# Optimization experiments

Hardware: AMD Instinct MI355X
Metric: run time of the kernel (lower is better)

## Reference

```python
import jax, jax.numpy as jnp
import numpy as np
from jax import lax

B, NP = 4, 8192          # events, points per event (equal-sized batches)
RATIO, R, K = 0.25, 0.2, 64
MP = int(NP * RATIO)     # sampled centers per event
D_IN = 32
BIG = 1e10


def _fps_one(pos):
    # Farthest point sampling (deterministic start at index 0). pos: [NP,3] -> [MP] int32
    d = jnp.sum((pos - pos[0]) ** 2, axis=-1)
    sel = jnp.zeros((MP,), jnp.int32)

    def body(i, carry):
        sel, d = carry
        nxt = jnp.argmax(d).astype(jnp.int32)
        sel = sel.at[i].set(nxt)
        d = jnp.minimum(d, jnp.sum((pos - pos[nxt]) ** 2, axis=-1))
        return sel, d

    sel, _ = lax.fori_loop(1, MP, body, (sel, d))
    return sel


def _ball_query_one(centers, pos):
    # centers: [MP,3], pos: [NP,3] -> neighbor idx [MP,K] int32, validity mask [MP,K]
    d2 = jnp.sum((centers[:, None, :] - pos[None, :, :]) ** 2, axis=-1)  # [MP,NP]
    d2m = jnp.where(d2 <= R * R, d2, BIG)
    neg, idx = lax.top_k(-d2m, K)          # K nearest within radius (deterministic)
    mask = (-neg) <= R * R
    return idx.astype(jnp.int32), mask


def reference(x, pos, batch, W1, b1, W2, b2, W3, b3):
    xb = x.reshape(B, NP, D_IN)
    pb = pos.reshape(B, NP, 3)

    sel = jax.vmap(_fps_one)(pb)                                   # [B,MP]
    centers = jnp.take_along_axis(pb, sel[..., None], axis=1)      # [B,MP,3]
    idx, mask = jax.vmap(_ball_query_one)(centers, pb)             # [B,MP,K]

    gather = jax.vmap(lambda a, i: a[i])
    pos_j = gather(pb, idx)                                        # [B,MP,K,3]
    x_j = gather(xb, idx)                                          # [B,MP,K,D_IN]

    rel = pos_j - centers[:, :, None, :]
    h = jnp.concatenate([x_j, rel], axis=-1)                       # [B,MP,K,D_IN+3]
    h = jax.nn.relu(h @ W1 + b1)
    h = jax.nn.relu(h @ W2 + b2)
    h = jax.nn.relu(h @ W3 + b3)                                   # [B,MP,K,128]

    h = jnp.where(mask[..., None], h, -BIG)
    x_out = jnp.max(h, axis=2).reshape(B * MP, -1)                 # max aggregation
    pos_out = centers.reshape(B * MP, 3)
    batch_out = jnp.repeat(jnp.arange(B, dtype=jnp.int32), MP)
    return x_out, pos_out, batch_out


def setup_inputs() -> dict:
    key = jax.random.key(0)
    ks = jax.random.split(key, 8)
    x = jax.random.normal(ks[0], (B * NP, D_IN), jnp.float32)
    pos = jax.random.uniform(ks[1], (B * NP, 3), jnp.float32)
    batch = (jnp.arange(B * NP) // NP).astype(jnp.int64)
    W1 = jax.random.normal(ks[2], (D_IN + 3, 64), jnp.float32) * 0.05
    b1 = jnp.zeros((64,), jnp.float32)
    W2 = jax.random.normal(ks[3], (64, 64), jnp.float32) * 0.05
    b2 = jnp.zeros((64,), jnp.float32)
    W3 = jax.random.normal(ks[4], (64, 128), jnp.float32) * 0.05
    b3 = jnp.zeros((128,), jnp.float32)
    return {"x": x, "pos": pos, "batch": batch, "W1": W1, "b1": b1,
            "W2": W2, "b2": b2, "W3": W3, "b3": b3}
```

## Files before the change

kernel.cpp:

```cpp
#include <hip/hip_runtime.h>


#define BATCH 4
#define NP 8192
#define MP 2048
#define KNN 64
#define DIN 32

#define DPP_FMAX(v, ctrl)                                                     \
  {                                                                           \
    int _t = __builtin_amdgcn_update_dpp(__float_as_int(v),                   \
                                         __float_as_int(v), (ctrl), 0xF,      \
                                         0xF, false);                         \
    (v) = fmaxf((v), __int_as_float(_t));                                     \
  }

typedef float v2f __attribute__((ext_vector_type(2)));

__global__ __launch_bounds__(1024) void fps_k(const float* __restrict__ pos,
                                              float* __restrict__ pout,
                                              float* __restrict__ bout)
{
  const int b = blockIdx.x;
  const int tid = threadIdx.x;
  const int lane = tid & 63, wid = tid >> 6;
  const float* __restrict__ pb = pos + (size_t)b * NP * 3;
  const int base = tid * 8;

  bout[b * MP + tid] = (float)b;
  bout[b * MP + 1024 + tid] = (float)b;

  __shared__ __align__(16) float ptab[NP * 3];
  __shared__ unsigned long long slt[2][16];

  float t[24];
  const float4* __restrict__ pv = (const float4*)(pb + (size_t)tid * 24);
#pragma unroll
  for (int q = 0; q < 6; q++) *(float4*)&t[q * 4] = pv[q];
#pragma unroll
  for (int q = 0; q < 6; q++) *(float4*)&ptab[tid * 24 + q * 4] = *(float4*)&t[q * 4];

  v2f px[4], py[4], pz[4], d[4];
#pragma unroll
  for (int j = 0; j < 4; j++) {
    px[j].x = t[6 * j + 0]; py[j].x = t[6 * j + 1]; pz[j].x = t[6 * j + 2];
    px[j].y = t[6 * j + 3]; py[j].y = t[6 * j + 4]; pz[j].y = t[6 * j + 5];
  }

  const float c0x = pb[0], c0y = pb[1], c0z = pb[2];
  if (tid == 0) {
    pout[(size_t)b * MP * 3 + 0] = c0x;
    pout[(size_t)b * MP * 3 + 1] = c0y;
    pout[(size_t)b * MP * 3 + 2] = c0z;
  }

  float bv = -1.f;
  {
    v2f cx = {c0x, c0x}, cy = {c0y, c0y}, cz = {c0z, c0z};
#pragma unroll
    for (int j = 0; j < 4; j++) {
      v2f dx = px[j] - cx, dy = py[j] - cy, dz = pz[j] - cz;
      v2f nd = dx * dx + dy * dy + dz * dz;
      d[j] = nd;
      bv = fmaxf(bv, fmaxf(nd.x, nd.y));
    }
  }

  for (int i = 1; i < MP; i++) {
    float v = bv;
    DPP_FMAX(v, 0x111);
    DPP_FMAX(v, 0x112);
    DPP_FMAX(v, 0x114);
    DPP_FMAX(v, 0x118);
    DPP_FMAX(v, 0x142);
    DPP_FMAX(v, 0x143);
    const float wmax =
        __int_as_float(__builtin_amdgcn_readlane(__float_as_int(v), 63));

    const unsigned long long m = __ballot(bv == wmax);
    const int src = (int)__builtin_ctzll(m);
    const int p = i & 1;
    if (lane == src) {
      int ks = 7;
#pragma unroll
      for (int k = 6; k >= 0; k--) {
        float dv = (k & 1) ? d[k >> 1].y : d[k >> 1].x;
        if (dv == wmax) ks = k;
      }
      slt[p][wid] = ((unsigned long long)__float_as_uint(wmax) << 32)
                    | (unsigned)(base + ks);
    }
    __syncthreads();

    const unsigned long long kv = slt[p][lane & 15];
    const float v2 = __uint_as_float((unsigned)(kv >> 32));
    float v2r = v2;
    DPP_FMAX(v2r, 0x111);
    DPP_FMAX(v2r, 0x112);
    DPP_FMAX(v2r, 0x114);
    DPP_FMAX(v2r, 0x118);
    const float mv =
        __int_as_float(__builtin_amdgcn_readlane(__float_as_int(v2r), 15));
    const unsigned long long m2 = __ballot(v2 == mv);
    const int mw = (int)__builtin_ctzll(m2);
    const int js = __builtin_amdgcn_readlane((int)(unsigned)kv, mw);
    const float ncx = ptab[js * 3 + 0];
    const float ncy = ptab[js * 3 + 1];
    const float ncz = ptab[js * 3 + 2];

    if (tid == 0) {
      pout[((size_t)b * MP + i) * 3 + 0] = ncx;
      pout[((size_t)b * MP + i) * 3 + 1] = ncy;
      pout[((size_t)b * MP + i) * 3 + 2] = ncz;
    }

    const v2f cx = {ncx, ncx}, cy = {ncy, ncy}, cz = {ncz, ncz};
    bv = -1.f;
#pragma unroll
    for (int j = 0; j < 4; j++) {
      v2f dx = px[j] - cx, dy = py[j] - cy, dz = pz[j] - cz;
      v2f nd = dx * dx + dy * dy + dz * dz;
      v2f dn;
      dn.x = fminf(d[j].x, nd.x);
      dn.y = fminf(d[j].y, nd.y);
      d[j] = dn;
      bv = fmaxf(bv, fmaxf(dn.x, dn.y));
    }
  }
}

__global__ __launch_bounds__(64) void ballq_k(const float* __restrict__ pos,
                                              const float* __restrict__ pout,
                                              int* __restrict__ nbr)
{
  const int wg = blockIdx.x;
  const int lane = threadIdx.x;
  const int b = wg >> 11;
  const float* __restrict__ pb = pos + (size_t)b * NP * 3;
  const float cx = pout[(size_t)wg * 3 + 0];
  const float cy = pout[(size_t)wg * 3 + 1];
  const float cz = pout[(size_t)wg * 3 + 2];
  const float R2 = (float)(0.2 * 0.2);

  __shared__ unsigned long long cand[1024];
  int cnt = 0;
  for (int basej = 0; basej < NP; basej += 64) {
    const int j = basej + lane;
    float dx = pb[j * 3 + 0] - cx;
    float dy = pb[j * 3 + 1] - cy;
    float dz = pb[j * 3 + 2] - cz;
    float d2 = dx * dx + dy * dy + dz * dz;
    bool in = (d2 <= R2);
    unsigned long long mb = __ballot(in);
    int pre = (int)__popcll(mb & ((1ull << lane) - 1ull));
    int slot = cnt + pre;
    if (in && slot < 1024)
      cand[slot] = ((unsigned long long)__float_as_uint(d2) << 32) | (unsigned int)j;
    cnt += (int)__popcll(mb);
  }
  if (cnt > 1024) cnt = 1024;

  int myout = -1;
  for (int r = 0; r < KNN; r++) {
    unsigned long long v = ~0ull; int slot = -1;
    for (int s = lane; s < cnt; s += 64) {
      unsigned long long c = cand[s];
      if (c < v) { v = c; slot = s; }
    }
#pragma unroll
    for (int off = 1; off < 64; off <<= 1) {
      unsigned long long ov = __shfl_xor(v, off);
      int os = __shfl_xor(slot, off);
      if (ov < v) { v = ov; slot = os; }
    }
    if (lane == r) myout = (v == ~0ull) ? -1 : (int)(v & 0xffffffffu);
    if (lane == 0 && slot >= 0) cand[slot] = ~0ull;
    __syncthreads();
  }
  nbr[(size_t)wg * KNN + lane] = myout;
}

__global__ __launch_bounds__(64) void p1_k(const float* __restrict__ x,
                                           const float* __restrict__ W1,
                                           float* __restrict__ P1)
{
  const int j = blockIdx.x;
  const int c = threadIdx.x;
  const float* __restrict__ xr = x + (size_t)j * DIN;
  float acc = 0.f;
#pragma unroll
  for (int k = 0; k < DIN; k++) acc += xr[k] * W1[k * 64 + c];
  P1[(size_t)j * 64 + c] = acc;
}

__global__ __launch_bounds__(256) void tw_k(const float* __restrict__ W2,
                                            const float* __restrict__ W3,
                                            float* __restrict__ W2T,
                                            float* __restrict__ W3T)
{
  int e = blockIdx.x * 256 + threadIdx.x;
  if (e < 64 * 64) {
    int c = e >> 6, k = e & 63;
    W2T[e] = W2[k * 64 + c];
  } else {
    int e2 = e - 64 * 64;
    if (e2 < 128 * 64) {
      int c = e2 >> 6, k = e2 & 63;
      W3T[e2] = W3[k * 128 + c];
    }
  }
}

__global__ __launch_bounds__(64) void mlp_k(const float* __restrict__ pos,
    const float* __restrict__ P1, const float* __restrict__ W1,
    const float* __restrict__ b1, const float* __restrict__ W2T,
    const float* __restrict__ b2, const float* __restrict__ W3T,
    const float* __restrict__ b3, const int* __restrict__ nbr,
    const float* __restrict__ pout, float* __restrict__ xout)
{
  __shared__ __align__(16) float h2s[64 * 68];
  const int wg = blockIdx.x;
  const int lane = threadIdx.x;
  const int b = wg >> 11;
  const int idx = nbr[(size_t)wg * KNN + lane];
  const bool valid = idx >= 0;
  const int j = valid ? idx : 0;
  const float cx = pout[(size_t)wg * 3 + 0];
  const float cy = pout[(size_t)wg * 3 + 1];
  const float cz = pout[(size_t)wg * 3 + 2];
  const float* __restrict__ pj = pos + ((size_t)b * NP + j) * 3;
  const float rx = pj[0] - cx, ry = pj[1] - cy, rz = pj[2] - cz;
  const float* __restrict__ p1r =
      (const float*)__builtin_assume_aligned(P1 + ((size_t)b * NP + j) * 64, 16);

  float h1[64];
#pragma unroll
  for (int k = 0; k < 64; k++) {
    float v = p1r[k] + rx * W1[32 * 64 + k] + ry * W1[33 * 64 + k]
                     + rz * W1[34 * 64 + k] + b1[k];
    h1[k] = fmaxf(v, 0.f);
  }

  for (int c4 = 0; c4 < 16; c4++) {
    float a0 = b2[c4 * 4 + 0], a1 = b2[c4 * 4 + 1];
    float a2 = b2[c4 * 4 + 2], a3 = b2[c4 * 4 + 3];
    const float* __restrict__ w0 = W2T + (c4 * 4 + 0) * 64;
    const float* __restrict__ w1 = W2T + (c4 * 4 + 1) * 64;
    const float* __restrict__ w2 = W2T + (c4 * 4 + 2) * 64;
    const float* __restrict__ w3 = W2T + (c4 * 4 + 3) * 64;
#pragma unroll
    for (int k = 0; k < 64; k++) {
      a0 += h1[k] * w0[k]; a1 += h1[k] * w1[k];
      a2 += h1[k] * w2[k]; a3 += h1[k] * w3[k];
    }
    float4 q;
    q.x = fmaxf(a0, 0.f); q.y = fmaxf(a1, 0.f);
    q.z = fmaxf(a2, 0.f); q.w = fmaxf(a3, 0.f);
    *(float4*)&h2s[lane * 68 + c4 * 4] = q;
  }

  float4 keep = make_float4(0.f, 0.f, 0.f, 0.f);
  const float* __restrict__ h2p = &h2s[lane * 68];
  for (int c4 = 0; c4 < 32; c4++) {
    float a0 = b3[c4 * 4 + 0], a1 = b3[c4 * 4 + 1];
    float a2 = b3[c4 * 4 + 2], a3 = b3[c4 * 4 + 3];
    const float* __restrict__ w0 = W3T + (c4 * 4 + 0) * 64;
    const float* __restrict__ w1 = W3T + (c4 * 4 + 1) * 64;
    const float* __restrict__ w2 = W3T + (c4 * 4 + 2) * 64;
    const float* __restrict__ w3 = W3T + (c4 * 4 + 3) * 64;
#pragma unroll
    for (int k4 = 0; k4 < 16; k4++) {
      float4 h = *(const float4*)&h2p[k4 * 4];
      a0 += h.x * w0[k4 * 4 + 0]; a0 += h.y * w0[k4 * 4 + 1];
      a0 += h.z * w0[k4 * 4 + 2]; a0 += h.w * w0[k4 * 4 + 3];
      a1 += h.x * w1[k4 * 4 + 0]; a1 += h.y * w1[k4 * 4 + 1];
      a1 += h.z * w1[k4 * 4 + 2]; a1 += h.w * w1[k4 * 4 + 3];
      a2 += h.x * w2[k4 * 4 + 0]; a2 += h.y * w2[k4 * 4 + 1];
      a2 += h.z * w2[k4 * 4 + 2]; a2 += h.w * w2[k4 * 4 + 3];
      a3 += h.x * w3[k4 * 4 + 0]; a3 += h.y * w3[k4 * 4 + 1];
      a3 += h.z * w3[k4 * 4 + 2]; a3 += h.w * w3[k4 * 4 + 3];
    }
    a0 = valid ? fmaxf(a0, 0.f) : 0.f;
    a1 = valid ? fmaxf(a1, 0.f) : 0.f;
    a2 = valid ? fmaxf(a2, 0.f) : 0.f;
    a3 = valid ? fmaxf(a3, 0.f) : 0.f;
#pragma unroll
    for (int off = 1; off < 64; off <<= 1) {
      a0 = fmaxf(a0, __shfl_xor(a0, off));
      a1 = fmaxf(a1, __shfl_xor(a1, off));
      a2 = fmaxf(a2, __shfl_xor(a2, off));
      a3 = fmaxf(a3, __shfl_xor(a3, off));
    }
    if (lane == c4) { keep.x = a0; keep.y = a1; keep.z = a2; keep.w = a3; }
  }
  if (lane < 32)
    *(float4*)&xout[(size_t)wg * 128 + lane * 4] = keep;
}

extern "C" void kernel_launch(void* const* d_in, const int* in_sizes, int n_in,
                              void* d_out, int out_size, void* d_ws, size_t ws_size,
                              hipStream_t stream)
{
  const float* x   = (const float*)d_in[0];
  const float* pos = (const float*)d_in[1];
  const float* W1 = (const float*)d_in[3];
  const float* b1 = (const float*)d_in[4];
  const float* W2 = (const float*)d_in[5];
  const float* b2 = (const float*)d_in[6];
  const float* W3 = (const float*)d_in[7];
  const float* b3 = (const float*)d_in[8];

  float* out  = (float*)d_out;
  float* xout = out;
  float* pout = out + 8192 * 128;
  float* bout = out + 8192 * 128 + 8192 * 3;

  char* ws = (char*)d_ws;
  float* P1  = (float*)ws;
  float* W2T = (float*)(ws + 8388608);
  float* W3T = (float*)(ws + 8404992);
  int*   nbr = (int*)(ws + 8437760);

  fps_k<<<dim3(BATCH), dim3(1024), 0, stream>>>(pos, pout, bout);
  p1_k<<<dim3(BATCH * NP), dim3(64), 0, stream>>>(x, W1, P1);
  tw_k<<<dim3(48), dim3(256), 0, stream>>>(W2, W3, W2T, W3T);
  ballq_k<<<dim3(BATCH * MP), dim3(64), 0, stream>>>(pos, pout, nbr);
  mlp_k<<<dim3(BATCH * MP), dim3(64), 0, stream>>>(pos, P1, W1, b1, W2T, b2,
                                                   W3T, b3, nbr, pout, xout);
}
```

Measured before the change: 2.554 ms.

## Fuse P1 and weight-transpose into FPS launch, carry coords through reductions

Folds the P1 projection and weight transpose kernels into extra blocks of the FPS launch, so they run concurrently with the four long serial FPS blocks instead of afterwards. The FPS loop no longer keeps a shared point table; the winning lane publishes its coordinates along with the max value, and readlane broadcasts them, which removes a dependent LDS lookup per iteration. An inline-asm v_max avoids NaN canonicalization in the DPP reductions. Ball query replaces the 64-bit shuffle reduction with two 32-bit DPP min reductions. Risks include different tie-breaking and the FPS blocks competing with the 2049 extra blocks for CUs.

```diff
diff --git a/kernel.cpp b/kernel.cpp
--- a/kernel.cpp
+++ b/kernel.cpp
@@ -7,22 +7,71 @@
 #define KNN 64
 #define DIN 32
 
+__device__ __forceinline__ float fmax_nc(float a, float b) {
+  float r;
+  asm("v_max_f32 %0, %1, %2" : "=v"(r) : "v"(a), "v"(b));
+  return r;
+}
+
 #define DPP_FMAX(v, ctrl)                                                     \
   {                                                                           \
     int _t = __builtin_amdgcn_update_dpp(__float_as_int(v),                   \
                                          __float_as_int(v), (ctrl), 0xF,      \
                                          0xF, false);                         \
-    (v) = fmaxf((v), __int_as_float(_t));                                     \
+    (v) = fmax_nc((v), __int_as_float(_t));                                   \
+  }
+
+#define DPP_MINU(v, ctrl)                                                     \
+  {                                                                           \
+    unsigned _t = (unsigned)__builtin_amdgcn_update_dpp((int)(v), (int)(v),   \
+                                                        (ctrl), 0xF, 0xF,    \
+                                                        false);               \
+    (v) = ((v) < _t) ? (v) : _t;                                              \
   }
 
 typedef float v2f __attribute__((ext_vector_type(2)));
 
 __global__ __launch_bounds__(1024) void fps_k(const float* __restrict__ pos,
+                                              const float* __restrict__ x,
+                                              const float* __restrict__ W1,
+                                              const float* __restrict__ W2,
+                                              const float* __restrict__ W3,
                                               float* __restrict__ pout,
-                                              float* __restrict__ bout)
+                                              float* __restrict__ bout,
+                                              float* __restrict__ P1,
+                                              float* __restrict__ W2T,
+                                              float* __restrict__ W3T)
 {
-  const int b = blockIdx.x;
+  const int bid = blockIdx.x;
   const int tid = threadIdx.x;
+
+  if (bid >= BATCH) {
+    if (bid < BATCH + 2048) {
+      const int j = (bid - BATCH) * 16 + (tid >> 6);
+      const int c = tid & 63;
+      const float* __restrict__ xr = x + (size_t)j * DIN;
+      float acc = 0.f;
+#pragma unroll
+      for (int k = 0; k < DIN; k++) acc += xr[k] * W1[k * 64 + c];
+      P1[(size_t)j * 64 + c] = acc;
+    } else {
+#pragma unroll
+      for (int it = 0; it < 12; it++) {
+        const int e = it * 1024 + tid;
+        if (e < 64 * 64) {
+          const int c = e >> 6, k = e & 63;
+          W2T[e] = W2[k * 64 + c];
+        } else {
+          const int e2 = e - 64 * 64;
+          const int c = e2 >> 6, k = e2 & 63;
+          W3T[e2] = W3[k * 128 + c];
+        }
+      }
+    }
+    return;
+  }
+
+  const int b = bid;
   const int lane = tid & 63, wid = tid >> 6;
   const float* __restrict__ pb = pos + (size_t)b * NP * 3;
   const int base = tid * 8;
@@ -30,15 +79,12 @@
   bout[b * MP + tid] = (float)b;
   bout[b * MP + 1024 + tid] = (float)b;
 
-  __shared__ __align__(16) float ptab[NP * 3];
-  __shared__ unsigned long long slt[2][16];
+  __shared__ __align__(16) float sc[2][16][4];
 
   float t[24];
   const float4* __restrict__ pv = (const float4*)(pb + (size_t)tid * 24);
 #pragma unroll
   for (int q = 0; q < 6; q++) *(float4*)&t[q * 4] = pv[q];
-#pragma unroll
-  for (int q = 0; q < 6; q++) *(float4*)&ptab[tid * 24 + q * 4] = *(float4*)&t[q * 4];
 
   v2f px[4], py[4], pz[4], d[4];
 #pragma unroll
@@ -56,13 +102,13 @@
 
   float bv = -1.f;
   {
-    v2f cx = {c0x, c0x}, cy = {c0y, c0y}, cz = {c0z, c0z};
+    const v2f cx = {c0x, c0x}, cy = {c0y, c0y}, cz = {c0z, c0z};
 #pragma unroll
     for (int j = 0; j < 4; j++) {
       v2f dx = px[j] - cx, dy = py[j] - cy, dz = pz[j] - cz;
       v2f nd = dx * dx + dy * dy + dz * dz;
       d[j] = nd;
-      bv = fmaxf(bv, fmaxf(nd.x, nd.y));
+      bv = fmaxf(fmaxf(nd.x, nd.y), bv);
     }
   }
 
@@ -81,19 +127,23 @@
     const int src = (int)__builtin_ctzll(m);
     const int p = i & 1;
     if (lane == src) {
-      int ks = 7;
+      float ox = px[3].y, oy = py[3].y, oz = pz[3].y;
 #pragma unroll
       for (int k = 6; k >= 0; k--) {
-        float dv = (k & 1) ? d[k >> 1].y : d[k >> 1].x;
-        if (dv == wmax) ks = k;
+        const float dv = (k & 1) ? d[k >> 1].y : d[k >> 1].x;
+        if (dv == wmax) {
+          ox = (k & 1) ? px[k >> 1].y : px[k >> 1].x;
+          oy = (k & 1) ? py[k >> 1].y : py[k >> 1].x;
+          oz = (k & 1) ? pz[k >> 1].y : pz[k >> 1].x;
+        }
       }
-      slt[p][wid] = ((unsigned long long)__float_as_uint(wmax) << 32)
-                    | (unsigned)(base + ks);
+      float4 q; q.x = ox; q.y = oy; q.z = oz; q.w = wmax;
+      *(float4*)&sc[p][wid][0] = q;
     }
     __syncthreads();
 
-    const unsigned long long kv = slt[p][lane & 15];
-    const float v2 = __uint_as_float((unsigned)(kv >> 32));
+    const float4 q = *(const float4*)&sc[p][lane & 15][0];
+    const float v2 = q.w;
     float v2r = v2;
     DPP_FMAX(v2r, 0x111);
     DPP_FMAX(v2r, 0x112);
@@ -103,10 +153,12 @@
         __int_as_float(__builtin_amdgcn_readlane(__float_as_int(v2r), 15));
     const unsigned long long m2 = __ballot(v2 == mv);
     const int mw = (int)__builtin_ctzll(m2);
-    const int js = __builtin_amdgcn_readlane((int)(unsigned)kv, mw);
-    const float ncx = ptab[js * 3 + 0];
-    const float ncy = ptab[js * 3 + 1];
-    const float ncz = ptab[js * 3 + 2];
+    const float ncx =
+        __int_as_float(__builtin_amdgcn_readlane(__float_as_int(q.x), mw));
+    const float ncy =
+        __int_as_float(__builtin_amdgcn_readlane(__float_as_int(q.y), mw));
+    const float ncz =
+        __int_as_float(__builtin_amdgcn_readlane(__float_as_int(q.z), mw));
 
     if (tid == 0) {
       pout[((size_t)b * MP + i) * 3 + 0] = ncx;
@@ -124,7 +176,7 @@
       dn.x = fminf(d[j].x, nd.x);
       dn.y = fminf(d[j].y, nd.y);
       d[j] = dn;
-      bv = fmaxf(bv, fmaxf(dn.x, dn.y));
+      bv = fmaxf(fmaxf(dn.x, dn.y), bv);
     }
   }
 }
@@ -167,48 +219,30 @@
       unsigned long long c = cand[s];
       if (c < v) { v = c; slot = s; }
     }
-#pragma unroll
-    for (int off = 1; off < 64; off <<= 1) {
-      unsigned long long ov = __shfl_xor(v, off);
-      int os = __shfl_xor(slot, off);
-      if (ov < v) { v = ov; slot = os; }
-    }
-    if (lane == r) myout = (v == ~0ull) ? -1 : (int)(v & 0xffffffffu);
-    if (lane == 0 && slot >= 0) cand[slot] = ~0ull;
+    const unsigned hi = (unsigned)(v >> 32);
+    unsigned h = hi;
+    DPP_MINU(h, 0x111);
+    DPP_MINU(h, 0x112);
+    DPP_MINU(h, 0x114);
+    DPP_MINU(h, 0x118);
+    DPP_MINU(h, 0x142);
+    DPP_MINU(h, 0x143);
+    const unsigned mb = (unsigned)__builtin_amdgcn_readlane((int)h, 63);
+    const unsigned jc = (hi == mb) ? (unsigned)(v & 0xffffffffu) : 0xffffffffu;
+    unsigned j2 = jc;
+    DPP_MINU(j2, 0x111);
+    DPP_MINU(j2, 0x112);
+    DPP_MINU(j2, 0x114);
+    DPP_MINU(j2, 0x118);
+    DPP_MINU(j2, 0x142);
+    DPP_MINU(j2, 0x143);
+    const unsigned jwin = (unsigned)__builtin_amdgcn_readlane((int)j2, 63);
+
+    if (lane == r) myout = (mb == 0xffffffffu) ? -1 : (int)jwin;
+    if (mb != 0xffffffffu && jc == jwin) cand[slot] = ~0ull;
     __syncthreads();
   }
   nbr[(size_t)wg * KNN + lane] = myout;
-}
-
-__global__ __launch_bounds__(64) void p1_k(const float* __restrict__ x,
-                                           const float* __restrict__ W1,
-                                           float* __restrict__ P1)
-{
-  const int j = blockIdx.x;
-  const int c = threadIdx.x;
-  const float* __restrict__ xr = x + (size_t)j * DIN;
-  float acc = 0.f;
-#pragma unroll
-  for (int k = 0; k < DIN; k++) acc += xr[k] * W1[k * 64 + c];
-  P1[(size_t)j * 64 + c] = acc;
-}
-
-__global__ __launch_bounds__(256) void tw_k(const float* __restrict__ W2,
-                                            const float* __restrict__ W3,
-                                            float* __restrict__ W2T,
-                                            float* __restrict__ W3T)
-{
-  int e = blockIdx.x * 256 + threadIdx.x;
-  if (e < 64 * 64) {
-    int c = e >> 6, k = e & 63;
-    W2T[e] = W2[k * 64 + c];
-  } else {
-    int e2 = e - 64 * 64;
-    if (e2 < 128 * 64) {
-      int c = e2 >> 6, k = e2 & 63;
-      W3T[e2] = W3[k * 128 + c];
-    }
-  }
 }
 
 __global__ __launch_bounds__(64) void mlp_k(const float* __restrict__ pos,
@@ -321,9 +355,8 @@
   float* W3T = (float*)(ws + 8404992);
   int*   nbr = (int*)(ws + 8437760);
 
-  fps_k<<<dim3(BATCH), dim3(1024), 0, stream>>>(pos, pout, bout);
-  p1_k<<<dim3(BATCH * NP), dim3(64), 0, stream>>>(x, W1, P1);
-  tw_k<<<dim3(48), dim3(256), 0, stream>>>(W2, W3, W2T, W3T);
+  fps_k<<<dim3(BATCH + 2048 + 1), dim3(1024), 0, stream>>>(
+      pos, x, W1, W2, W3, pout, bout, P1, W2T, W3T);
   ballq_k<<<dim3(BATCH * MP), dim3(64), 0, stream>>>(pos, pout, nbr);
   mlp_k<<<dim3(BATCH * MP), dim3(64), 0, stream>>>(pos, P1, W1, b1, W2T, b2,
                                                    W3T, b3, nbr, pout, xout);
```

Measured after the change: 2.590 ms. No clear change (+1.4%).
